# Performance work log

Measured on AMD Instinct MI355X. Metric: run time of the kernel, lower is better.

## Reference

```python
import jax, jax.numpy as jnp
import numpy as np

B, T, D, U, O = 256, 512, 256, 512, 64  # batch, n_steps, feature_in, units, n_output


def setup_inputs() -> dict:
    key = jax.random.key(0)
    k_x, k_wx, k_wh, k_wd = jax.random.split(key, 4)
    x = jax.random.normal(k_x, (B, T, D), dtype=jnp.float32)
    # Lecun-normal-ish init scales so activations stay sane
    Wx = jax.random.normal(k_wx, (D, 4 * U), dtype=jnp.float32) * (1.0 / np.sqrt(D))
    Wh = jax.random.normal(k_wh, (U, 4 * U), dtype=jnp.float32) * (1.0 / np.sqrt(U))
    b = jnp.zeros((4 * U,), dtype=jnp.float32)
    Wd = jax.random.normal(k_wd, (U, O), dtype=jnp.float32) * (1.0 / np.sqrt(U))
    bd = jnp.zeros((O,), dtype=jnp.float32)
    return {"x": x, "Wx": Wx, "Wh": Wh, "b": b, "Wd": Wd, "bd": bd}


def reference(x, Wx, Wh, b, Wd, bd):
    """Sequential LSTM scan (flax nn.LSTMCell math) + per-step dense decode.

    x: [B, T, D] -> y: [B, T, O]
    """
    batch = x.shape[0]
    units = Wh.shape[0]
    c0 = jnp.zeros((batch, units), dtype=x.dtype)
    h0 = jnp.zeros((batch, units), dtype=x.dtype)

    def step(carry, xt):
        c, h = carry
        gates = xt @ Wx + h @ Wh + b            # [B, 4U]
        i, f, g, o = jnp.split(gates, 4, axis=-1)
        i = jax.nn.sigmoid(i)
        f = jax.nn.sigmoid(f)
        g = jnp.tanh(g)
        o = jax.nn.sigmoid(o)
        c_new = f * c + i * g
        h_new = o * jnp.tanh(c_new)
        y = h_new @ Wd + bd                     # [B, O]
        return (c_new, h_new), y

    xs = jnp.swapaxes(x, 0, 1)                  # [T, B, D]
    _, ys = jax.lax.scan(step, (c0, h0), xs)    # ys: [T, B, O]
    return jnp.swapaxes(ys, 0, 1)               # [B, T, O]
```

## Files before the change

kernel.cpp:

```cpp
#include <hip/hip_runtime.h>
#include <hip/hip_bf16.h>


#define Bb 256
#define Tt 512
#define Dd 256
#define Uu 512
#define Oo 64

typedef short bs8 __attribute__((ext_vector_type(8)));
typedef float f32x4 __attribute__((ext_vector_type(4)));

__device__ __forceinline__ unsigned short f2bf(float f) {
  unsigned u = __float_as_uint(f);
  u += 0x7fffu + ((u >> 16) & 1u);
  return (unsigned short)(u >> 16);
}
__device__ __forceinline__ unsigned f2bf2(float lo, float hi) {
  union { __hip_bfloat162 b; unsigned u; } cv;
  cv.b = __float22bfloat162_rn(make_float2(lo, hi));
  return cv.u;
}
__device__ __forceinline__ float sigm(float v) { return 1.0f / (1.0f + __expf(-v)); }
__device__ __forceinline__ float tanhfast(float v) { return 2.0f / (1.0f + __expf(-2.0f * v)) - 1.0f; }

__device__ __forceinline__ int zbyte(int row, int k) {
  return (row * 1536 + k * 2) ^ ((row & 7) << 4);
}

__global__ void rnn_init_bar(unsigned* bar) {
  for (int i = threadIdx.x; i < 16 * 32 * 32; i += 256)
    __hip_atomic_store(&bar[i], 0u, __ATOMIC_RELAXED, __HIP_MEMORY_SCOPE_AGENT);
}

__launch_bounds__(256, 2)
__global__ void rnn_lstm_kernel(const float* __restrict__ x, const float* __restrict__ Wx,
                                const float* __restrict__ Wh, const float* __restrict__ bias,
                                const float* __restrict__ Wd, const float* __restrict__ bd,
                                float* __restrict__ out, unsigned short* hbuf, unsigned* bar) {
  __shared__ __align__(16) char zs[16 * 768 * 2];
  __shared__ float gates[4][16][17];
  __shared__ float yp[4][16][2];

  const int tid = threadIdx.x;
  const int lane = tid & 63;
  const int wid = tid >> 6;
  const int bid = blockIdx.x;
  const int bg = (bid & 7) | ((bid >> 8) << 3);
  const int ug = (bid >> 3) & 31;
  const int b_base = bg * 16;
  const int u_base = ug * 16;
  const int oc0 = ug * 2;

  unsigned* fl = bar + bg * 32 * 32;

  bs8 breg[24];
  {
    const int gc = wid * 512 + u_base + (lane & 15);
    const int kfr = (lane >> 4) * 8;
#pragma unroll
    for (int ks = 0; ks < 24; ++ks) {
      bs8 bb;
#pragma unroll
      for (int e = 0; e < 8; ++e) {
        int kg = ks * 32 + kfr + e;
        float w = (kg < 256) ? Wx[(size_t)kg * 2048 + gc]
                             : Wh[(size_t)(kg - 256) * 2048 + gc];
        bb[e] = (short)f2bf(w);
      }
      breg[ks] = bb;
    }
  }
  bs8 wdfrag[4];
  {
    const int col = lane & 15;
    const int kfr = (lane >> 4) * 8;
#pragma unroll
    for (int i = 0; i < 4; ++i) {
      int ksl = wid * 4 + i;
      bs8 bb;
#pragma unroll
      for (int e = 0; e < 8; ++e) {
        int u = ksl * 32 + kfr + e;
        bb[e] = (col < 2) ? (short)f2bf(Wd[(size_t)u * Oo + oc0 + col]) : (short)0;
      }
      wdfrag[i] = bb;
    }
  }

  const int prow = tid & 15;
  const int us4 = (tid >> 4) & 3;
  float bi[4], bff[4], bgg[4], boo[4];
  if (tid < 64) {
#pragma unroll
    for (int j = 0; j < 4; ++j) {
      int ugl = u_base + us4 * 4 + j;
      bi[j]  = bias[0 * 512 + ugl];
      bff[j] = bias[1 * 512 + ugl];
      bgg[j] = bias[2 * 512 + ugl];
      boo[j] = bias[3 * 512 + ugl];
    }
  }
  float cst[4] = {0.f, 0.f, 0.f, 0.f};

  union U16 { unsigned long long q[2]; bs8 v; };

  {
    int row = tid >> 4;
    int d0 = (tid & 15) * 16;
    const float* xp = x + ((size_t)(b_base + row) * Tt + 0) * Dd + d0;
    float4 v0 = *(const float4*)xp;
    float4 v1 = *(const float4*)(xp + 4);
    float4 v2 = *(const float4*)(xp + 8);
    float4 v3 = *(const float4*)(xp + 12);
    uint4 p0, p1;
    p0.x = f2bf2(v0.x, v0.y); p0.y = f2bf2(v0.z, v0.w);
    p0.z = f2bf2(v1.x, v1.y); p0.w = f2bf2(v1.z, v1.w);
    p1.x = f2bf2(v2.x, v2.y); p1.y = f2bf2(v2.z, v2.w);
    p1.z = f2bf2(v3.x, v3.y); p1.w = f2bf2(v3.z, v3.w);
    *(uint4*)(zs + zbyte(row, d0)) = p0;
    *(uint4*)(zs + zbyte(row, d0 + 8)) = p1;
  }
#pragma unroll
  for (int i = 0; i < 4; ++i) {
    int c = tid + i * 256;
    int row = c >> 6;
    int u0 = (c & 63) * 8;
    bs8 zz = {0, 0, 0, 0, 0, 0, 0, 0};
    *(bs8*)(zs + zbyte(row, 256 + u0)) = zz;
  }
  __syncthreads();

  const int arow = lane & 15;
  const int akf = (lane >> 4) * 8;
  const int rb = (lane >> 4) * 4;

  for (int t = 0; t < Tt; ++t) {
    float4 xv0, xv1, xv2, xv3;
    const int xrow = tid >> 4;
    const int xd0 = (tid & 15) * 16;
    if (t + 1 < Tt) {
      const float* xp = x + ((size_t)(b_base + xrow) * Tt + (t + 1)) * Dd + xd0;
      xv0 = *(const float4*)xp;
      xv1 = *(const float4*)(xp + 4);
      xv2 = *(const float4*)(xp + 8);
      xv3 = *(const float4*)(xp + 12);
    }

    f32x4 acc0 = {0, 0, 0, 0}, acc1 = {0, 0, 0, 0};
#pragma unroll
    for (int ks = 0; ks < 24; ks += 2) {
      bs8 av0 = *(const bs8*)(zs + zbyte(arow, ks * 32 + akf));
      bs8 av1 = *(const bs8*)(zs + zbyte(arow, (ks + 1) * 32 + akf));
      acc0 = __builtin_amdgcn_mfma_f32_16x16x32_bf16(av0, breg[ks], acc0, 0, 0, 0);
      acc1 = __builtin_amdgcn_mfma_f32_16x16x32_bf16(av1, breg[ks + 1], acc1, 0, 0, 0);
    }
    acc0 += acc1;
    {
      f32x4 yacc = {0, 0, 0, 0};
#pragma unroll
      for (int i = 0; i < 4; ++i) {
        int ks = 8 + wid * 4 + i;
        bs8 av = *(const bs8*)(zs + zbyte(arow, ks * 32 + akf));
        yacc = __builtin_amdgcn_mfma_f32_16x16x32_bf16(av, wdfrag[i], yacc, 0, 0, 0);
      }
      if ((lane & 15) < 2) {
#pragma unroll
        for (int j = 0; j < 4; ++j) yp[wid][rb + j][lane & 15] = yacc[j];
      }
    }
    {
      const int u16 = lane & 15;
#pragma unroll
      for (int j = 0; j < 4; ++j) gates[wid][rb + j][u16] = acc0[j];
    }
    __syncthreads();

    if (tid < 64) {
      float hv[4];
#pragma unroll
      for (int j = 0; j < 4; ++j) {
        int u = us4 * 4 + j;
        float gi = gates[0][prow][u] + bi[j];
        float gf = gates[1][prow][u] + bff[j];
        float gg = gates[2][prow][u] + bgg[j];
        float go = gates[3][prow][u] + boo[j];
        float iv = sigm(gi), fv = sigm(gf), gv = tanhfast(gg), ov = sigm(go);
        float cn = fv * cst[j] + iv * gv;
        cst[j] = cn;
        hv[j] = ov * tanhfast(cn);
      }
      unsigned long long hpack =
          (unsigned long long)f2bf2(hv[0], hv[1]) |
          ((unsigned long long)f2bf2(hv[2], hv[3]) << 32);
      unsigned long long* hp =
          (unsigned long long*)(hbuf + (size_t)(t & 1) * Bb * Uu +
                                (size_t)(b_base + prow) * Uu + u_base + us4 * 4);
      unsigned long long old = __hip_atomic_exchange(hp, hpack, __ATOMIC_RELAXED,
                                                     __HIP_MEMORY_SCOPE_AGENT);
      asm volatile("" :: "v"(old));
    } else if (t > 0 && tid >= 128 && tid < 160) {
      int b = (tid - 128) >> 1, oc = tid & 1;
      float s = bd[oc0 + oc] + yp[0][b][oc] + yp[1][b][oc] + yp[2][b][oc] + yp[3][b][oc];
      out[((size_t)(b_base + b) * Tt + (t - 1)) * Oo + oc0 + oc] = s;
    }
    __syncthreads();
    if (tid == 0) {
      unsigned oldf = __hip_atomic_exchange(&fl[ug * 32], (unsigned)(t + 1),
                                            __ATOMIC_RELAXED, __HIP_MEMORY_SCOPE_AGENT);
      asm volatile("" :: "v"(oldf));
    }

    if (t + 1 < Tt) {
      uint4 p0, p1;
      p0.x = f2bf2(xv0.x, xv0.y); p0.y = f2bf2(xv0.z, xv0.w);
      p0.z = f2bf2(xv1.x, xv1.y); p0.w = f2bf2(xv1.z, xv1.w);
      p1.x = f2bf2(xv2.x, xv2.y); p1.y = f2bf2(xv2.z, xv2.w);
      p1.z = f2bf2(xv3.x, xv3.y); p1.w = f2bf2(xv3.z, xv3.w);
      *(uint4*)(zs + zbyte(xrow, xd0)) = p0;
      *(uint4*)(zs + zbyte(xrow, xd0 + 8)) = p1;
    }
    if (wid == 1) {
      for (;;) {
        unsigned v = __hip_atomic_load(&fl[(lane & 31) * 32], __ATOMIC_RELAXED,
                                       __HIP_MEMORY_SCOPE_AGENT);
        if (!__any((int)(v < (unsigned)(t + 1)))) break;
        __builtin_amdgcn_s_sleep(2);
      }
    }
    __builtin_amdgcn_sched_barrier(0);
    __syncthreads();

    {
      const unsigned short* hsrc = hbuf + (size_t)(t & 1) * Bb * Uu;
#pragma unroll
      for (int i = 0; i < 4; ++i) {
        int c = tid + i * 256;
        int row = c >> 6;
        int u0 = (c & 63) * 8;
        const unsigned long long* p =
            (const unsigned long long*)(hsrc + (size_t)(b_base + row) * Uu + u0);
        U16 uu;
        uu.q[0] = __hip_atomic_load(p, __ATOMIC_RELAXED, __HIP_MEMORY_SCOPE_AGENT);
        uu.q[1] = __hip_atomic_load(p + 1, __ATOMIC_RELAXED, __HIP_MEMORY_SCOPE_AGENT);
        *(bs8*)(zs + zbyte(row, 256 + u0)) = uu.v;
      }
    }
    __syncthreads();
  }

  {
    f32x4 yacc = {0, 0, 0, 0};
#pragma unroll
    for (int i = 0; i < 4; ++i) {
      int ks = 8 + wid * 4 + i;
      bs8 av = *(const bs8*)(zs + zbyte(arow, ks * 32 + akf));
      yacc = __builtin_amdgcn_mfma_f32_16x16x32_bf16(av, wdfrag[i], yacc, 0, 0, 0);
    }
    if ((lane & 15) < 2) {
#pragma unroll
      for (int j = 0; j < 4; ++j) yp[wid][rb + j][lane & 15] = yacc[j];
    }
    __syncthreads();
    if (tid < 32) {
      int b = tid >> 1, oc = tid & 1;
      float s = bd[oc0 + oc] + yp[0][b][oc] + yp[1][b][oc] + yp[2][b][oc] + yp[3][b][oc];
      out[((size_t)(b_base + b) * Tt + (Tt - 1)) * Oo + oc0 + oc] = s;
    }
  }
}

extern "C" void kernel_launch(void* const* d_in, const int* in_sizes, int n_in,
                              void* d_out, int out_size, void* d_ws, size_t ws_size,
                              hipStream_t stream) {
  const float* x  = (const float*)d_in[0];
  const float* Wx = (const float*)d_in[1];
  const float* Wh = (const float*)d_in[2];
  const float* bs = (const float*)d_in[3];
  const float* Wd = (const float*)d_in[4];
  const float* bd = (const float*)d_in[5];
  float* out = (float*)d_out;

  unsigned short* hbuf = (unsigned short*)d_ws;
  unsigned* bar = (unsigned*)((char*)d_ws + (size_t)2 * Bb * Uu * 2);

  rnn_init_bar<<<1, 256, 0, stream>>>(bar);
  rnn_lstm_kernel<<<dim3(512), dim3(256), 0, stream>>>(x, Wx, Wh, bs, Wd, bd, out, hbuf, bar);
}
```

Before: 2.691 ms.

## Process two batch groups per block to overlap one group's barrier wait with the other's compute

Each block now handles two 16-row batch groups (A and B) that share the same register-resident gate weights, so the grid halves to 256 blocks at one block per CU. The step loop interleaves the groups: while group A's flag is published and its peers catch up, group B's MFMA and pointwise work runs, so cross-block sync latency is hidden behind useful compute. The output projection moves from MFMA with a mostly zero-padded weight fragment to a scalar FP32 dot product using Wd staged in LDS. The risks are lower occupancy, more LDS, a longer serial chain per step, and a more intricate polling order.

```diff
diff --git a/kernel.cpp b/kernel.cpp
--- a/kernel.cpp
+++ b/kernel.cpp
@@ -21,6 +21,9 @@
   cv.b = __float22bfloat162_rn(make_float2(lo, hi));
   return cv.u;
 }
+__device__ __forceinline__ float bf2f(unsigned short s) {
+  return __uint_as_float(((unsigned)s) << 16);
+}
 __device__ __forceinline__ float sigm(float v) { return 1.0f / (1.0f + __expf(-v)); }
 __device__ __forceinline__ float tanhfast(float v) { return 2.0f / (1.0f + __expf(-2.0f * v)) - 1.0f; }
 
@@ -33,26 +36,28 @@
     __hip_atomic_store(&bar[i], 0u, __ATOMIC_RELAXED, __HIP_MEMORY_SCOPE_AGENT);
 }
 
-__launch_bounds__(256, 2)
+__launch_bounds__(256, 1)
 __global__ void rnn_lstm_kernel(const float* __restrict__ x, const float* __restrict__ Wx,
                                 const float* __restrict__ Wh, const float* __restrict__ bias,
                                 const float* __restrict__ Wd, const float* __restrict__ bd,
                                 float* __restrict__ out, unsigned short* hbuf, unsigned* bar) {
-  __shared__ __align__(16) char zs[16 * 768 * 2];
-  __shared__ float gates[4][16][17];
-  __shared__ float yp[4][16][2];
+  __shared__ __align__(16) char zsA[16 * 768 * 2];
+  __shared__ __align__(16) char zsB[16 * 768 * 2];
+  __shared__ float gatesA[4][16][17], gatesB[4][16][17];
+  __shared__ float wdl[512][2];
+  __shared__ float ypA[16][2][16], ypB[16][2][16];
 
   const int tid = threadIdx.x;
   const int lane = tid & 63;
   const int wid = tid >> 6;
   const int bid = blockIdx.x;
-  const int bg = (bid & 7) | ((bid >> 8) << 3);
-  const int ug = (bid >> 3) & 31;
-  const int b_base = bg * 16;
+  const int bgA = bid & 7, bgB = bgA + 8;
+  const int ug = bid >> 3;
+  const int bbA = bgA * 16, bbB = bgB * 16;
   const int u_base = ug * 16;
   const int oc0 = ug * 2;
-
-  unsigned* fl = bar + bg * 32 * 32;
+  unsigned* flA = bar + bgA * 32 * 32;
+  unsigned* flB = bar + bgB * 32 * 32;
 
   bs8 breg[24];
   {
@@ -71,25 +76,10 @@
       breg[ks] = bb;
     }
   }
-  bs8 wdfrag[4];
-  {
-    const int col = lane & 15;
-    const int kfr = (lane >> 4) * 8;
-#pragma unroll
-    for (int i = 0; i < 4; ++i) {
-      int ksl = wid * 4 + i;
-      bs8 bb;
-#pragma unroll
-      for (int e = 0; e < 8; ++e) {
-        int u = ksl * 32 + kfr + e;
-        bb[e] = (col < 2) ? (short)f2bf(Wd[(size_t)u * Oo + oc0 + col]) : (short)0;
-      }
-      wdfrag[i] = bb;
-    }
-  }
 
   const int prow = tid & 15;
-  const int us4 = (tid >> 4) & 3;
+  const int usec = tid >> 4;
+  const int us4 = usec & 3;
   float bi[4], bff[4], bgg[4], boo[4];
   if (tid < 64) {
 #pragma unroll
@@ -101,173 +91,175 @@
       boo[j] = bias[3 * 512 + ugl];
     }
   }
-  float cst[4] = {0.f, 0.f, 0.f, 0.f};
-
-  union U16 { unsigned long long q[2]; bs8 v; };
-
-  {
-    int row = tid >> 4;
-    int d0 = (tid & 15) * 16;
-    const float* xp = x + ((size_t)(b_base + row) * Tt + 0) * Dd + d0;
-    float4 v0 = *(const float4*)xp;
-    float4 v1 = *(const float4*)(xp + 4);
-    float4 v2 = *(const float4*)(xp + 8);
-    float4 v3 = *(const float4*)(xp + 12);
-    uint4 p0, p1;
-    p0.x = f2bf2(v0.x, v0.y); p0.y = f2bf2(v0.z, v0.w);
-    p0.z = f2bf2(v1.x, v1.y); p0.w = f2bf2(v1.z, v1.w);
-    p1.x = f2bf2(v2.x, v2.y); p1.y = f2bf2(v2.z, v2.w);
-    p1.z = f2bf2(v3.x, v3.y); p1.w = f2bf2(v3.z, v3.w);
-    *(uint4*)(zs + zbyte(row, d0)) = p0;
-    *(uint4*)(zs + zbyte(row, d0 + 8)) = p1;
-  }
+  float cstA[4] = {0.f, 0.f, 0.f, 0.f};
+  float cstB[4] = {0.f, 0.f, 0.f, 0.f};
+
+#pragma unroll
+  for (int i = 0; i < 4; ++i) {
+    int c = tid + i * 256;
+    int u = c >> 1, oc = c & 1;
+    wdl[u][oc] = Wd[(size_t)u * Oo + oc0 + oc];
+  }
+
+#define XSTAGE(ZS, BB, TIDX) do {                                              \
+    int row_ = tid >> 4; int d0_ = (tid & 15) * 16;                            \
+    const float* xp_ = x + ((size_t)((BB) + row_) * Tt + (TIDX)) * Dd + d0_;   \
+    float4 v0_ = *(const float4*)xp_;  float4 v1_ = *(const float4*)(xp_ + 4); \
+    float4 v2_ = *(const float4*)(xp_ + 8); float4 v3_ = *(const float4*)(xp_ + 12);\
+    uint4 p0_, p1_;                                                            \
+    p0_.x = f2bf2(v0_.x, v0_.y); p0_.y = f2bf2(v0_.z, v0_.w);                  \
+    p0_.z = f2bf2(v1_.x, v1_.y); p0_.w = f2bf2(v1_.z, v1_.w);                  \
+    p1_.x = f2bf2(v2_.x, v2_.y); p1_.y = f2bf2(v2_.z, v2_.w);                  \
+    p1_.z = f2bf2(v3_.x, v3_.y); p1_.w = f2bf2(v3_.z, v3_.w);                  \
+    *(uint4*)((ZS) + zbyte(row_, d0_)) = p0_;                                  \
+    *(uint4*)((ZS) + zbyte(row_, d0_ + 8)) = p1_;                              \
+  } while (0)
+
+#define MFMA_PHASE(ZS, GATES) do {                                             \
+    f32x4 a0_ = {0, 0, 0, 0}, a1_ = {0, 0, 0, 0};                              \
+    _Pragma("unroll")                                                          \
+    for (int ks = 0; ks < 24; ks += 2) {                                       \
+      bs8 av0_ = *(const bs8*)((ZS) + zbyte(arow, ks * 32 + akf));             \
+      bs8 av1_ = *(const bs8*)((ZS) + zbyte(arow, (ks + 1) * 32 + akf));       \
+      a0_ = __builtin_amdgcn_mfma_f32_16x16x32_bf16(av0_, breg[ks], a0_, 0, 0, 0); \
+      a1_ = __builtin_amdgcn_mfma_f32_16x16x32_bf16(av1_, breg[ks + 1], a1_, 0, 0, 0); \
+    }                                                                          \
+    a0_ += a1_;                                                                \
+    { const int u16_ = lane & 15; const int rb_ = (lane >> 4) * 4;             \
+      _Pragma("unroll")                                                        \
+      for (int j = 0; j < 4; ++j) (GATES)[wid][rb_ + j][u16_] = a0_[j]; }      \
+  } while (0)
+
+#define PW_SWAP(GATES, CST, BB) do {                                           \
+    float hv_[4];                                                              \
+    _Pragma("unroll")                                                          \
+    for (int j = 0; j < 4; ++j) {                                              \
+      int u_ = us4 * 4 + j;                                                    \
+      float gi_ = (GATES)[0][prow][u_] + bi[j];                                \
+      float gf_ = (GATES)[1][prow][u_] + bff[j];                               \
+      float gg_ = (GATES)[2][prow][u_] + bgg[j];                               \
+      float go_ = (GATES)[3][prow][u_] + boo[j];                               \
+      float iv_ = sigm(gi_), fv_ = sigm(gf_), gv_ = tanhfast(gg_), ov_ = sigm(go_); \
+      float cn_ = fv_ * (CST)[j] + iv_ * gv_; (CST)[j] = cn_;                  \
+      hv_[j] = ov_ * tanhfast(cn_);                                            \
+    }                                                                          \
+    unsigned long long hp_ = (unsigned long long)f2bf2(hv_[0], hv_[1]) |       \
+        ((unsigned long long)f2bf2(hv_[2], hv_[3]) << 32);                     \
+    unsigned long long* pp_ = (unsigned long long*)(hbuf + (size_t)(t & 1) * Bb * Uu \
+        + (size_t)((BB) + prow) * Uu + u_base + us4 * 4);                      \
+    unsigned long long old_ = __hip_atomic_exchange(pp_, hp_, __ATOMIC_RELAXED,\
+        __HIP_MEMORY_SCOPE_AGENT);                                             \
+    asm volatile("" :: "v"(old_));                                             \
+  } while (0)
+
+#define YDECODE(ZS, YP) do {                                                   \
+    float s0_ = 0.f, s1_ = 0.f;                                                \
+    _Pragma("unroll")                                                          \
+    for (int c8 = 0; c8 < 4; ++c8) {                                           \
+      int k_ = 256 + usec * 32 + c8 * 8;                                       \
+      bs8 hv_ = *(const bs8*)((ZS) + zbyte(prow, k_));                         \
+      _Pragma("unroll")                                                        \
+      for (int e = 0; e < 8; ++e) {                                            \
+        float hf_ = bf2f((unsigned short)hv_[e]);                              \
+        int u_ = usec * 32 + c8 * 8 + e;                                       \
+        s0_ += hf_ * wdl[u_][0]; s1_ += hf_ * wdl[u_][1];                      \
+      }                                                                        \
+    }                                                                          \
+    (YP)[prow][0][usec] = s0_; (YP)[prow][1][usec] = s1_;                      \
+  } while (0)
+
+#define FLAGPUB(FL) do {                                                       \
+    unsigned oldf_ = __hip_atomic_exchange(&(FL)[ug * 32], (unsigned)(t + 1),  \
+        __ATOMIC_RELAXED, __HIP_MEMORY_SCOPE_AGENT);                           \
+    asm volatile("" :: "v"(oldf_));                                            \
+  } while (0)
+
+#define POLL(FL) do {                                                          \
+    for (;;) {                                                                 \
+      unsigned v_ = __hip_atomic_load(&(FL)[(lane & 31) * 32],                 \
+          __ATOMIC_RELAXED, __HIP_MEMORY_SCOPE_AGENT);                         \
+      if (!__any((int)(v_ < (unsigned)(t + 1)))) break;                        \
+      __builtin_amdgcn_s_sleep(2);                                             \
+    }                                                                          \
+  } while (0)
+
+#define HLOAD(ZS, BB) do {                                                     \
+    const unsigned short* hs_ = hbuf + (size_t)(t & 1) * Bb * Uu;              \
+    int idx_ = (tid < 64) ? tid : tid - 64;         \
+    for (int c_ = idx_; c_ < 1024; c_ += 192) {                                \
+      int row_ = c_ >> 6; int u0_ = (c_ & 63) * 8;                             \
+      const unsigned long long* p_ = (const unsigned long long*)               \
+          (hs_ + (size_t)((BB) + row_) * Uu + u0_);                            \
+      unsigned long long q0_ = __hip_atomic_load(p_, __ATOMIC_RELAXED, __HIP_MEMORY_SCOPE_AGENT); \
+      unsigned long long q1_ = __hip_atomic_load(p_ + 1, __ATOMIC_RELAXED, __HIP_MEMORY_SCOPE_AGENT); \
+      *(unsigned long long*)((ZS) + zbyte(row_, 256 + u0_)) = q0_;             \
+      *(unsigned long long*)((ZS) + zbyte(row_, 256 + u0_ + 4)) = q1_;         \
+    }                                                                          \
+  } while (0)
+
+#define YSTORE(YP, BB, TT) do {                                                \
+    int b_ = lane >> 1, oc_ = lane & 1;                                        \
+    float s_ = bd[oc0 + oc_];                                                  \
+    _Pragma("unroll")                                                          \
+    for (int q_ = 0; q_ < 16; ++q_) s_ += (YP)[b_][oc_][q_];                   \
+    out[((size_t)((BB) + b_) * Tt + (TT)) * Oo + oc0 + oc_] = s_;              \
+  } while (0)
+
+  XSTAGE(zsA, bbA, 0);
+  XSTAGE(zsB, bbB, 0);
 #pragma unroll
   for (int i = 0; i < 4; ++i) {
     int c = tid + i * 256;
     int row = c >> 6;
     int u0 = (c & 63) * 8;
     bs8 zz = {0, 0, 0, 0, 0, 0, 0, 0};
-    *(bs8*)(zs + zbyte(row, 256 + u0)) = zz;
+    *(bs8*)(zsA + zbyte(row, 256 + u0)) = zz;
+    *(bs8*)(zsB + zbyte(row, 256 + u0)) = zz;
   }
   __syncthreads();
 
   const int arow = lane & 15;
   const int akf = (lane >> 4) * 8;
-  const int rb = (lane >> 4) * 4;
 
   for (int t = 0; t < Tt; ++t) {
-    float4 xv0, xv1, xv2, xv3;
-    const int xrow = tid >> 4;
-    const int xd0 = (tid & 15) * 16;
-    if (t + 1 < Tt) {
-      const float* xp = x + ((size_t)(b_base + xrow) * Tt + (t + 1)) * Dd + xd0;
-      xv0 = *(const float4*)xp;
-      xv1 = *(const float4*)(xp + 4);
-      xv2 = *(const float4*)(xp + 8);
-      xv3 = *(const float4*)(xp + 12);
-    }
-
-    f32x4 acc0 = {0, 0, 0, 0}, acc1 = {0, 0, 0, 0};
-#pragma unroll
-    for (int ks = 0; ks < 24; ks += 2) {
-      bs8 av0 = *(const bs8*)(zs + zbyte(arow, ks * 32 + akf));
-      bs8 av1 = *(const bs8*)(zs + zbyte(arow, (ks + 1) * 32 + akf));
-      acc0 = __builtin_amdgcn_mfma_f32_16x16x32_bf16(av0, breg[ks], acc0, 0, 0, 0);
-      acc1 = __builtin_amdgcn_mfma_f32_16x16x32_bf16(av1, breg[ks + 1], acc1, 0, 0, 0);
-    }
-    acc0 += acc1;
-    {
-      f32x4 yacc = {0, 0, 0, 0};
-#pragma unroll
-      for (int i = 0; i < 4; ++i) {
-        int ks = 8 + wid * 4 + i;
-        bs8 av = *(const bs8*)(zs + zbyte(arow, ks * 32 + akf));
-        yacc = __builtin_amdgcn_mfma_f32_16x16x32_bf16(av, wdfrag[i], yacc, 0, 0, 0);
-      }
-      if ((lane & 15) < 2) {
-#pragma unroll
-        for (int j = 0; j < 4; ++j) yp[wid][rb + j][lane & 15] = yacc[j];
-      }
-    }
-    {
-      const int u16 = lane & 15;
-#pragma unroll
-      for (int j = 0; j < 4; ++j) gates[wid][rb + j][u16] = acc0[j];
-    }
-    __syncthreads();
-
-    if (tid < 64) {
-      float hv[4];
-#pragma unroll
-      for (int j = 0; j < 4; ++j) {
-        int u = us4 * 4 + j;
-        float gi = gates[0][prow][u] + bi[j];
-        float gf = gates[1][prow][u] + bff[j];
-        float gg = gates[2][prow][u] + bgg[j];
-        float go = gates[3][prow][u] + boo[j];
-        float iv = sigm(gi), fv = sigm(gf), gv = tanhfast(gg), ov = sigm(go);
-        float cn = fv * cst[j] + iv * gv;
-        cst[j] = cn;
-        hv[j] = ov * tanhfast(cn);
-      }
-      unsigned long long hpack =
-          (unsigned long long)f2bf2(hv[0], hv[1]) |
-          ((unsigned long long)f2bf2(hv[2], hv[3]) << 32);
-      unsigned long long* hp =
-          (unsigned long long*)(hbuf + (size_t)(t & 1) * Bb * Uu +
-                                (size_t)(b_base + prow) * Uu + u_base + us4 * 4);
-      unsigned long long old = __hip_atomic_exchange(hp, hpack, __ATOMIC_RELAXED,
-                                                     __HIP_MEMORY_SCOPE_AGENT);
-      asm volatile("" :: "v"(old));
-    } else if (t > 0 && tid >= 128 && tid < 160) {
-      int b = (tid - 128) >> 1, oc = tid & 1;
-      float s = bd[oc0 + oc] + yp[0][b][oc] + yp[1][b][oc] + yp[2][b][oc] + yp[3][b][oc];
-      out[((size_t)(b_base + b) * Tt + (t - 1)) * Oo + oc0 + oc] = s;
-    }
-    __syncthreads();
-    if (tid == 0) {
-      unsigned oldf = __hip_atomic_exchange(&fl[ug * 32], (unsigned)(t + 1),
-                                            __ATOMIC_RELAXED, __HIP_MEMORY_SCOPE_AGENT);
-      asm volatile("" :: "v"(oldf));
-    }
-
-    if (t + 1 < Tt) {
-      uint4 p0, p1;
-      p0.x = f2bf2(xv0.x, xv0.y); p0.y = f2bf2(xv0.z, xv0.w);
-      p0.z = f2bf2(xv1.x, xv1.y); p0.w = f2bf2(xv1.z, xv1.w);
-      p1.x = f2bf2(xv2.x, xv2.y); p1.y = f2bf2(xv2.z, xv2.w);
-      p1.z = f2bf2(xv3.x, xv3.y); p1.w = f2bf2(xv3.z, xv3.w);
-      *(uint4*)(zs + zbyte(xrow, xd0)) = p0;
-      *(uint4*)(zs + zbyte(xrow, xd0 + 8)) = p1;
-    }
-    if (wid == 1) {
-      for (;;) {
-        unsigned v = __hip_atomic_load(&fl[(lane & 31) * 32], __ATOMIC_RELAXED,
-                                       __HIP_MEMORY_SCOPE_AGENT);
-        if (!__any((int)(v < (unsigned)(t + 1)))) break;
-        __builtin_amdgcn_s_sleep(2);
-      }
-    }
+    MFMA_PHASE(zsA, gatesA);
+    __syncthreads();
+    if (tid < 64) PW_SWAP(gatesA, cstA, bbA);
+    if (t + 1 < Tt) XSTAGE(zsA, bbA, t + 1);
+    if (t > 0) YDECODE(zsA, ypA);
+    __syncthreads();
+    if (tid == 0) FLAGPUB(flA);
+    MFMA_PHASE(zsB, gatesB);
+    __syncthreads();
+    if (tid < 64) PW_SWAP(gatesB, cstB, bbB);
+    if (t + 1 < Tt) XSTAGE(zsB, bbB, t + 1);
+    if (t > 0) YDECODE(zsB, ypB);
+    if (wid == 1) POLL(flA);
     __builtin_amdgcn_sched_barrier(0);
     __syncthreads();
-
-    {
-      const unsigned short* hsrc = hbuf + (size_t)(t & 1) * Bb * Uu;
-#pragma unroll
-      for (int i = 0; i < 4; ++i) {
-        int c = tid + i * 256;
-        int row = c >> 6;
-        int u0 = (c & 63) * 8;
-        const unsigned long long* p =
-            (const unsigned long long*)(hsrc + (size_t)(b_base + row) * Uu + u0);
-        U16 uu;
-        uu.q[0] = __hip_atomic_load(p, __ATOMIC_RELAXED, __HIP_MEMORY_SCOPE_AGENT);
-        uu.q[1] = __hip_atomic_load(p + 1, __ATOMIC_RELAXED, __HIP_MEMORY_SCOPE_AGENT);
-        *(bs8*)(zs + zbyte(row, 256 + u0)) = uu.v;
-      }
-    }
-    __syncthreads();
-  }
-
-  {
-    f32x4 yacc = {0, 0, 0, 0};
-#pragma unroll
-    for (int i = 0; i < 4; ++i) {
-      int ks = 8 + wid * 4 + i;
-      bs8 av = *(const bs8*)(zs + zbyte(arow, ks * 32 + akf));
-      yacc = __builtin_amdgcn_mfma_f32_16x16x32_bf16(av, wdfrag[i], yacc, 0, 0, 0);
-    }
-    if ((lane & 15) < 2) {
-#pragma unroll
-      for (int j = 0; j < 4; ++j) yp[wid][rb + j][lane & 15] = yacc[j];
-    }
-    __syncthreads();
-    if (tid < 32) {
-      int b = tid >> 1, oc = tid & 1;
-      float s = bd[oc0 + oc] + yp[0][b][oc] + yp[1][b][oc] + yp[2][b][oc] + yp[3][b][oc];
-      out[((size_t)(b_base + b) * Tt + (Tt - 1)) * Oo + oc0 + oc] = s;
-    }
-  }
+    if (tid == 0) FLAGPUB(flB);
+    if (wid != 1) {
+      HLOAD(zsA, bbA);
+    } else {
+      POLL(flB);
+      if (t > 0 && lane < 32) YSTORE(ypA, bbA, t - 1);
+    }
+    __builtin_amdgcn_sched_barrier(0);
+    __syncthreads();
+    if (wid != 1) {
+      HLOAD(zsB, bbB);
+    } else {
+      if (t > 0 && lane < 32) YSTORE(ypB, bbB, t - 1);
+    }
+    __syncthreads();
+  }
+
+  YDECODE(zsA, ypA);
+  __syncthreads();
+  if (tid < 64 && lane < 32) YSTORE(ypA, bbA, Tt - 1);
+  YDECODE(zsB, ypB);
+  __syncthreads();
+  if (tid < 64 && lane < 32) YSTORE(ypB, bbB, Tt - 1);
 }
 
 extern "C" void kernel_launch(void* const* d_in, const int* in_sizes, int n_in,
@@ -285,5 +277,5 @@
   unsigned* bar = (unsigned*)((char*)d_ws + (size_t)2 * Bb * Uu * 2);
 
   rnn_init_bar<<<1, 256, 0, stream>>>(bar);
-  rnn_lstm_kernel<<<dim3(512), dim3(256), 0, stream>>>(x, Wx, Wh, bs, Wd, bd, out, hbuf, bar);
-}
+  rnn_lstm_kernel<<<dim3(256), dim3(256), 0, stream>>>(x, Wx, Wh, bs, Wd, bd, out, hbuf, bar);
+}
```

Measured after the change: 4.605 ms. +71.1%, slower.
